# Kernel tuning notes

Measured on AMD Instinct MI355X. Metric: run time of the kernel, lower is better.

Reference implementation:

```python
import math
import jax, jax.numpy as jnp
import numpy as np

B, S, DIM, H = 16, 1024, 1024, 16
HD = DIM // H            # head_dim = 64
ROPE_DIM = HD // 2       # 32; per-axis rotary dim
FT = 32                  # ft_seq_len, FT*FT == S
PT = 16                  # pt_seq_len
THETA = 10000.0
EPS = 1e-6


def _rope_cos_sin():
    # freqs_for='lang'
    freqs = 1.0 / THETA ** (jnp.arange(0, ROPE_DIM, 2, dtype=jnp.float32) / ROPE_DIM)  # [ROPE_DIM//2]
    t = jnp.arange(FT, dtype=jnp.float32) / FT * PT                                    # [FT]
    fs = jnp.einsum('n,f->nf', t, freqs)                                               # [FT, ROPE_DIM//2]
    fs = jnp.repeat(fs, 2, axis=-1)                                                    # [FT, ROPE_DIM]
    fh = jnp.broadcast_to(fs[:, None, :], (FT, FT, ROPE_DIM))
    fw = jnp.broadcast_to(fs[None, :, :], (FT, FT, ROPE_DIM))
    f = jnp.concatenate([fh, fw], axis=-1).reshape(-1, 2 * ROPE_DIM)                   # [S, HD]
    return jnp.cos(f), jnp.sin(f)


def _rotate_half(x):
    x1, x2 = jnp.split(x, 2, axis=-1)
    return jnp.concatenate((-x2, x1), axis=-1)


def _rms_norm(x, w):
    xf = x.astype(jnp.float32)
    var = jnp.mean(jnp.square(xf), axis=-1, keepdims=True)
    return (w * (xf * jax.lax.rsqrt(var + EPS))).astype(x.dtype)


def setup_inputs() -> dict:
    key = jax.random.key(0)
    ks = jax.random.split(key, 4)
    sd = 1.0 / math.sqrt(DIM)
    return {
        'x': jax.random.normal(ks[0], (B, S, DIM), dtype=jnp.float32),
        'w_qkv': jax.random.normal(ks[1], (DIM, 3 * DIM), dtype=jnp.float32) * sd,
        'b_qkv': jnp.zeros((3 * DIM,), dtype=jnp.float32),
        'q_norm_w': jnp.ones((HD,), dtype=jnp.float32),
        'k_norm_w': jnp.ones((HD,), dtype=jnp.float32),
        'w_out': jax.random.normal(ks[2], (DIM, DIM), dtype=jnp.float32) * sd,
        'b_out': jnp.zeros((DIM,), dtype=jnp.float32),
    }


def reference(x, w_qkv, b_qkv, q_norm_w, k_norm_w, w_out, b_out):
    cos, sin = _rope_cos_sin()                    # [S, HD] each
    cos = cos[None, None].astype(x.dtype)
    sin = sin[None, None].astype(x.dtype)

    qkv = x @ w_qkv + b_qkv                       # [B,S,3*DIM]
    qkv = qkv.reshape(B, S, 3, H, HD).transpose(2, 0, 3, 1, 4)  # [3,B,H,S,HD]
    q, k, v = qkv[0], qkv[1], qkv[2]

    q = _rms_norm(q, q_norm_w)
    k = _rms_norm(k, k_norm_w)

    q = q * cos + _rotate_half(q) * sin
    k = k * cos + _rotate_half(k) * sin

    scale = 1.0 / math.sqrt(HD)
    logits = jnp.einsum('bhqd,bhkd->bhqk', q.astype(jnp.float32), k.astype(jnp.float32)) * scale
    attn = jax.nn.softmax(logits, axis=-1).astype(x.dtype)
    out = jnp.einsum('bhqk,bhkd->bhqd', attn, v)  # [B,H,S,HD]

    out = out.transpose(0, 2, 1, 3).reshape(B, S, DIM)
    return out @ w_out + b_out
```

## Files before the change

### kernel.cpp

```cpp
#include <hip/hip_runtime.h>
#include <cstdint>
#include <cstddef>

#define B_    16
#define S_    1024
#define DIM_  1024
#define H_    16
#define HD_   64
#define TDIM  3072

typedef unsigned short ushort_t;
typedef unsigned int   uint_t;
typedef __attribute__((ext_vector_type(8)))  short s8v;
typedef __attribute__((ext_vector_type(4)))  float f32x4;
typedef __attribute__((ext_vector_type(16))) float f32x16;

__device__ __forceinline__ float b2f(ushort_t u) {
    union { uint_t i; float f; } t; t.i = (uint_t)u << 16; return t.f;
}
__device__ __forceinline__ ushort_t f2b(float f) {
    union { float f; uint_t i; } t; t.f = f;
    uint_t r = t.i + 0x7FFFu + ((t.i >> 16) & 1u);
    return (ushort_t)(r >> 16);
}
__device__ __forceinline__ uint_t cvt_pk_bf16(float a, float b) {
    uint_t r;
    asm("v_cvt_pk_bf16_f32 %0, %1, %2" : "=v"(r) : "v"(a), "v"(b));
    return r;
}
__device__ __forceinline__ float max3f(float a, float b, float c) {
    float r;
    asm("v_max3_f32 %0, %1, %2, %3" : "=v"(r) : "v"(a), "v"(b), "v"(c));
    return r;
}

__device__ __forceinline__ f32x4 mfma_bf16(s8v a, s8v b, f32x4 c) {
    asm volatile("v_mfma_f32_16x16x32_bf16 %0, %1, %2, %0" : "+v"(c) : "v"(a), "v"(b));
    return c;
}
__device__ __forceinline__ f32x16 mfma32_bf16(s8v a, s8v b, f32x16 c) {
    asm volatile("v_mfma_f32_32x32x16_bf16 %0, %1, %2, %0" : "+v"(c) : "v"(a), "v"(b));
    return c;
}

__device__ __forceinline__ void gload16(const void* g, void* l) {
    __builtin_amdgcn_global_load_lds(
        (const __attribute__((address_space(1))) uint_t*)g,
        (__attribute__((address_space(3))) uint_t*)l, 16, 0, 0);
}

__device__ __forceinline__ void bar() {
    asm volatile("" ::: "memory");
    __builtin_amdgcn_s_barrier();
    asm volatile("" ::: "memory");
}
__device__ __forceinline__ void wait_vm0() {
    asm volatile("s_waitcnt vmcnt(0)" ::: "memory");
}
__device__ __forceinline__ void wait_vm4() {
    asm volatile("s_waitcnt vmcnt(4)" ::: "memory");
}

__global__ __launch_bounds__(256) void f32_to_bf16_vec(const float* __restrict__ src,
                                                       short* __restrict__ dst, int n8) {
    int i = blockIdx.x * 256 + threadIdx.x;
    if (i < n8) {
        float4 a = *(const float4*)(src + (size_t)i * 8);
        float4 b = *(const float4*)(src + (size_t)i * 8 + 4);
        s8v t;
        t[0] = (short)f2b(a.x); t[1] = (short)f2b(a.y);
        t[2] = (short)f2b(a.z); t[3] = (short)f2b(a.w);
        t[4] = (short)f2b(b.x); t[5] = (short)f2b(b.y);
        t[6] = (short)f2b(b.z); t[7] = (short)f2b(b.w);
        *(s8v*)(dst + (size_t)i * 8) = t;
    }
}

__global__ __launch_bounds__(256) void rope_tables(float* __restrict__ cos_t,
                                                   float* __restrict__ sin_t) {
    int idx = blockIdx.x * 256 + threadIdx.x;
    int s = idx >> 6;
    int d = idx & 63;
    int pos = (d < 32) ? (s >> 5) : (s & 31);
    int i   = (d & 31) >> 1;
    float freq  = expf(-(float)i * 0.5756462732485115f);
    float angle = (float)pos * 0.5f * freq;
    cos_t[idx] = cosf(angle);
    sin_t[idx] = sinf(angle);
}

__global__ __launch_bounds__(256) void transpose_to_bf16(const float* __restrict__ Wsrc,
                                                         short* __restrict__ WT,
                                                         int K, int N) {
    __shared__ float t[32][33];
    int tx = threadIdx.x & 31, ty = threadIdx.x >> 5;
    int n0 = blockIdx.x * 32, k0 = blockIdx.y * 32;
#pragma unroll
    for (int i = 0; i < 4; ++i)
        t[ty + 8 * i][tx] = Wsrc[(size_t)(k0 + ty + 8 * i) * N + n0 + tx];
    __syncthreads();
#pragma unroll
    for (int i = 0; i < 4; ++i)
        WT[(size_t)(n0 + ty + 8 * i) * K + k0 + tx] = (short)f2b(t[tx][ty + 8 * i]);
}

template<typename CT, bool NORM>
__global__ __launch_bounds__(512) void gemm8ph(
        const short* __restrict__ A, const short* __restrict__ BT,
        const float* __restrict__ bias, CT* __restrict__ C,
        int M, int N, int K, int NX,
        const float* __restrict__ qw, const float* __restrict__ kw,
        const float* __restrict__ cos_t, const float* __restrict__ sin_t) {
    __shared__ short As[2][256 * 64];
    __shared__ short Bs[3][256 * 64];

    const int tid  = threadIdx.x;
    const int w    = tid >> 6;
    const int lane = tid & 63;
    const int l15  = lane & 15, lg = lane >> 4;
    const int wm = w >> 2, wn = w & 3;

    const int nwg  = gridDim.x;
    const int cpx  = nwg >> 3;
    const int wgid = (blockIdx.x & 7) * cpx + (blockIdx.x >> 3);
    const int bx = wgid % NX, by = wgid / NX;
    const int m0 = by * 256, n0 = bx * 256;

    const int NT = K >> 6;

    const int sgrow = w * 8 + (lane >> 3);
    const int ksrc  = (((lane & 7) ^ (lane >> 3)) * 8);

    auto stageA = [&](int t, int buf) {
        const size_t k0 = (size_t)t * 64;
#pragma unroll
        for (int j = 0; j < 4; ++j)
            gload16(A + (size_t)(m0 + j * 64 + sgrow) * K + k0 + ksrc,
                    &As[buf][(j * 64 + w * 8) * 64]);
    };
    auto stageB = [&](int t, int buf) {
        const size_t k0 = (size_t)t * 64;
#pragma unroll
        for (int j = 0; j < 4; ++j)
            gload16(BT + (size_t)(n0 + j * 64 + sgrow) * K + k0 + ksrc,
                    &Bs[buf][(j * 64 + w * 8) * 64]);
    };

    const int swz = l15 & 7;

    auto rdA = [&](int buf, int mh, s8v (&dst)[4][2]) {
#pragma unroll
        for (int i = 0; i < 4; ++i) {
            int row = wm * 128 + mh * 64 + i * 16 + l15;
#pragma unroll
            for (int kk = 0; kk < 2; ++kk)
                dst[i][kk] = *(const s8v*)&As[buf][row * 64 + (((kk * 4 + lg) ^ swz) * 8)];
        }
    };
    auto rdB = [&](int buf, int nh, s8v (&dst)[4][2]) {
#pragma unroll
        for (int ni = 0; ni < 2; ++ni) {
            int row = wn * 64 + (nh * 2 + ni) * 16 + l15;
#pragma unroll
            for (int kk = 0; kk < 2; ++kk)
                dst[nh * 2 + ni][kk] = *(const s8v*)&Bs[buf][row * 64 + (((kk * 4 + lg) ^ swz) * 8)];
        }
    };

    stageA(0, 0);
    stageB(0, 0);
    stageB(1, 1);
    wait_vm4();
    bar();

    s8v a0[4][2], a1[4][2], bb[4][2];
    rdA(0, 0, a0);
    rdB(0, 0, bb);
    rdB(0, 1, bb);
    rdA(0, 1, a1);

    f32x4 acc[8][4] = {};

    int bufB = 0;
    for (int t = 0; t < NT; ++t) {
        const int bufA  = t & 1;
        const int nbufB = (bufB == 2) ? 0 : bufB + 1;
        const int sbufB = (nbufB == 2) ? 0 : nbufB + 1;

        if (t + 1 < NT) stageA(t + 1, bufA ^ 1);
        if (t + 2 < NT) stageB(t + 2, sbufB);

        __builtin_amdgcn_s_setprio(1);
#pragma unroll
        for (int i = 0; i < 4; ++i)
#pragma unroll
            for (int ni = 0; ni < 2; ++ni)
#pragma unroll
                for (int kk = 0; kk < 2; ++kk)
                    acc[i][ni] = mfma_bf16(a0[i][kk], bb[ni][kk], acc[i][ni]);
        __builtin_amdgcn_s_setprio(0);

        __builtin_amdgcn_s_setprio(1);
#pragma unroll
        for (int i = 0; i < 4; ++i)
#pragma unroll
            for (int ni = 2; ni < 4; ++ni)
#pragma unroll
                for (int kk = 0; kk < 2; ++kk)
                    acc[i][ni] = mfma_bf16(a0[i][kk], bb[ni][kk], acc[i][ni]);
        __builtin_amdgcn_s_setprio(0);

        __builtin_amdgcn_s_setprio(1);
#pragma unroll
        for (int i = 0; i < 4; ++i)
#pragma unroll
            for (int ni = 0; ni < 2; ++ni)
#pragma unroll
                for (int kk = 0; kk < 2; ++kk)
                    acc[4 + i][ni] = mfma_bf16(a1[i][kk], bb[ni][kk], acc[4 + i][ni]);
        __builtin_amdgcn_s_setprio(0);

        if (t < NT - 2) wait_vm4(); else wait_vm0();
        bar();

        if (t + 1 < NT) {
            rdA(bufA ^ 1, 0, a0);
            rdB(nbufB, 0, bb);
        }

        __builtin_amdgcn_s_setprio(1);
#pragma unroll
        for (int i = 0; i < 4; ++i)
#pragma unroll
            for (int ni = 2; ni < 4; ++ni)
#pragma unroll
                for (int kk = 0; kk < 2; ++kk)
                    acc[4 + i][ni] = mfma_bf16(a1[i][kk], bb[ni][kk], acc[4 + i][ni]);
        __builtin_amdgcn_s_setprio(0);

        if (t + 1 < NT) {
            rdB(nbufB, 1, bb);
            rdA(bufA ^ 1, 1, a1);
        }
        bufB = nbufB;
    }

    const int colbase = n0 + wn * 64;
    if constexpr (NORM) {
        if (colbase < 2048) {
            const float* nw = (colbase < 1024) ? qw : kw;
            float wv[4], bv[4];
#pragma unroll
            for (int ni = 0; ni < 4; ++ni) {
                wv[ni] = nw[16 * ni + l15];
                bv[ni] = bias[colbase + 16 * ni + l15];
            }
#pragma unroll
            for (int mi = 0; mi < 8; ++mi) {
#pragma unroll
                for (int r = 0; r < 4; ++r) {
                    int row = m0 + wm * 128 + mi * 16 + lg * 4 + r;
                    int s = row & (S_ - 1);
                    float v[4];
#pragma unroll
                    for (int ni = 0; ni < 4; ++ni) v[ni] = acc[mi][ni][r] + bv[ni];
                    float ss = v[0]*v[0] + v[1]*v[1] + v[2]*v[2] + v[3]*v[3];
                    ss += __shfl_xor(ss, 1);
                    ss += __shfl_xor(ss, 2);
                    ss += __shfl_xor(ss, 4);
                    ss += __shfl_xor(ss, 8);
                    float rms = rsqrtf(ss * (1.0f / 64.0f) + 1e-6f);
                    float xn[4];
#pragma unroll
                    for (int ni = 0; ni < 4; ++ni) xn[ni] = v[ni] * rms * wv[ni];
#pragma unroll
                    for (int ni = 0; ni < 4; ++ni) {
                        int d = 16 * ni + l15;
                        float c  = cos_t[s * 64 + d];
                        float sn = sin_t[s * 64 + d];
                        float rot = (ni < 2) ? -xn[ni + 2] : xn[ni - 2];
                        C[(size_t)row * N + colbase + d] = (short)f2b(xn[ni] * c + rot * sn);
                    }
                }
            }
            return;
        }
    }
#pragma unroll
    for (int ni = 0; ni < 4; ++ni) {
        float bvv = bias[colbase + 16 * ni + l15];
#pragma unroll
        for (int mi = 0; mi < 8; ++mi) {
#pragma unroll
            for (int r = 0; r < 4; ++r) {
                size_t row = (size_t)(m0 + wm * 128 + mi * 16 + lg * 4 + r);
                int    col = colbase + 16 * ni + l15;
                float v = acc[mi][ni][r] + bvv;
                if constexpr (sizeof(CT) == 4) C[row * N + col] = v;
                else                           C[row * N + col] = (short)f2b(v);
            }
        }
    }
}

__global__ __launch_bounds__(256) void attn_mfma(const short* __restrict__ qkv,
                                                 short* __restrict__ attn) {
    __shared__ ushort_t pool[9216];
    ushort_t* Ks = pool;
    ushort_t* Vt = pool + 4608;

    const float SC  = 0.18033688011112042f;
    const float THR = 11.0f;

    const int tid  = threadIdx.x;
    const int w    = tid >> 6;
    const int lane = tid & 63;
    const int l31  = lane & 31, l5 = lane >> 5;

    const int bid = blockIdx.x;
    const int xcd = bid & 7;
    const int jj_ = bid >> 3;
    const int bh  = xcd * 32 + (jj_ & 31);
    const int b   = bh >> 4, h = bh & 15;
    const int q0  = (jj_ >> 5) * 128;

    const short* qbase = qkv + (size_t)b * S_ * TDIM + h * HD_;
    const short* kb_ = qbase + DIM_;
    const short* vb_ = qbase + 2 * DIM_;

    s8v qf[4];
#pragma unroll
    for (int kc = 0; kc < 4; ++kc)
        qf[kc] = *(const s8v*)(qbase + (size_t)(q0 + w * 32 + l31) * TDIM + kc * 16 + l5 * 8);

    f32x16 of0 = {}, of1 = {};
    float m_s = -1e30f, l_s = 0.f;

    const int kr   = tid >> 3;
    const int kp8  = (tid & 7) * 8;
    const int vkp  = tid >> 3;
    const int va   = tid & 7;
    const int vp8  = va * 8;
    const int k2    = 2 * vkp;
    const int kperm = (k2 & 0x33) | ((k2 & 4) << 1) | ((k2 & 8) >> 1);
    const int vcol  = kperm ^ ((va & 3) << 4);
    const int vsw   = ((l31 >> 3) & 3) << 4;

    s8v kA, kB, vA, vB;
    auto prefetch = [&](int kt) {
        const short* kbt = kb_ + (size_t)kt * 64 * TDIM;
        const short* vbt = vb_ + (size_t)kt * 64 * TDIM;
        kA = *(const s8v*)(kbt + (size_t)kr * TDIM + kp8);
        kB = *(const s8v*)(kbt + (size_t)(kr + 32) * TDIM + kp8);
        vA = *(const s8v*)(vbt + (size_t)k2 * TDIM + vp8);
        vB = *(const s8v*)(vbt + (size_t)(k2 + 1) * TDIM + vp8);
    };
    prefetch(0);

    for (int kt = 0; kt < 16; ++kt) {
        *(s8v*)&Ks[kr * 72 + kp8]        = kA;
        *(s8v*)&Ks[(kr + 32) * 72 + kp8] = kB;
#pragma unroll
        for (int j = 0; j < 8; ++j) {
            uint_t pk = (ushort_t)vA[j] | ((uint_t)(ushort_t)vB[j] << 16);
            *(uint_t*)&Vt[(vp8 + j) * 72 + vcol] = pk;
        }
        __syncthreads();

        if (kt < 15) prefetch(kt + 1);

        f32x16 st0 = {}, st1 = {};
        __builtin_amdgcn_s_setprio(1);
#pragma unroll
        for (int kc = 0; kc < 4; ++kc) {
            s8v kf0 = *(const s8v*)&Ks[l31 * 72 + kc * 16 + l5 * 8];
            s8v kf1 = *(const s8v*)&Ks[(32 + l31) * 72 + kc * 16 + l5 * 8];
            st0 = mfma32_bf16(kf0, qf[kc], st0);
            st1 = mfma32_bf16(kf1, qf[kc], st1);
        }
        __builtin_amdgcn_s_setprio(0);

        float ma = fmaxf(st0[0], st1[0]);
        float mb = fmaxf(st0[8], st1[8]);
#pragma unroll
        for (int r = 1; r < 8; ++r) {
            ma = max3f(st0[r],     st1[r],     ma);
            mb = max3f(st0[8 + r], st1[8 + r], mb);
        }
        float mx = fmaxf(ma, mb);
        mx = fmaxf(mx, __shfl_xor(mx, 32));
        float mxs = mx * SC;

        if (!__all(mxs <= m_s + THR)) {
            float mnew  = fmaxf(m_s, mxs);
            float alpha = exp2f(m_s - mnew);
            m_s = mnew;
            l_s *= alpha;
#pragma unroll
            for (int r = 0; r < 16; ++r) { of0[r] *= alpha; of1[r] *= alpha; }
        }

        float la = 0.f, lb = 0.f, lc = 0.f, ld = 0.f;
#pragma unroll
        for (int r = 0; r < 16; r += 2) {
            float p00 = exp2f(__builtin_fmaf(st0[r],     SC, -m_s));
            float p01 = exp2f(__builtin_fmaf(st0[r + 1], SC, -m_s));
            float p10 = exp2f(__builtin_fmaf(st1[r],     SC, -m_s));
            float p11 = exp2f(__builtin_fmaf(st1[r + 1], SC, -m_s));
            st0[r] = p00; st0[r + 1] = p01;
            st1[r] = p10; st1[r + 1] = p11;
            la += p00; lb += p01; lc += p10; ld += p11;
        }
        float ls = (la + lb) + (lc + ld);
        ls += __shfl_xor(ls, 32);
        l_s += ls;

        uint_t P20[8], P21[8];
#pragma unroll
        for (int i = 0; i < 8; ++i) {
            P20[i] = cvt_pk_bf16(st0[2 * i], st0[2 * i + 1]);
            P21[i] = cvt_pk_bf16(st1[2 * i], st1[2 * i + 1]);
        }

        __builtin_amdgcn_s_setprio(1);
#pragma unroll
        for (int kb = 0; kb < 2; ++kb) {
            const uint_t* P2 = kb ? P21 : P20;
#pragma unroll
            for (int c = 0; c < 2; ++c) {
                union { uint_t u[4]; s8v v; } pf;
                pf.u[0] = P2[4 * c + 0];
                pf.u[1] = P2[4 * c + 1];
                pf.u[2] = P2[4 * c + 2];
                pf.u[3] = P2[4 * c + 3];

                int kcol = (kb * 32 + c * 16 + l5 * 8) ^ vsw;
                s8v vf0 = *(const s8v*)&Vt[l31 * 72 + kcol];
                s8v vf1 = *(const s8v*)&Vt[(32 + l31) * 72 + kcol];
                of0 = mfma32_bf16(vf0, pf.v, of0);
                of1 = mfma32_bf16(vf1, pf.v, of1);
            }
        }
        __builtin_amdgcn_s_setprio(0);
        __syncthreads();
    }

    float inv = 1.0f / l_s;
    ushort_t* OL = pool + w * 2304;
#pragma unroll
    for (int r = 0; r < 16; ++r) {
        int d = (r & 3) + 8 * (r >> 2) + 4 * l5;
        OL[l31 * 72 + d]      = f2b(of0[r] * inv);
        OL[l31 * 72 + 32 + d] = f2b(of1[r] * inv);
    }
#pragma unroll
    for (int i = 0; i < 4; ++i) {
        int idx = lane + i * 64;
        int row = idx >> 3, ch = idx & 7;
        *(s8v*)&attn[((size_t)b * S_ + q0 + w * 32 + row) * DIM_ + h * HD_ + ch * 8] =
            *(const s8v*)&OL[row * 72 + ch * 8];
    }
}

extern "C" void kernel_launch(void* const* d_in, const int* in_sizes, int n_in,
                              void* d_out, int out_size, void* d_ws, size_t ws_size,
                              hipStream_t stream) {
    const float* x        = (const float*)d_in[0];
    const float* w_qkv    = (const float*)d_in[1];
    const float* b_qkv    = (const float*)d_in[2];
    const float* q_norm_w = (const float*)d_in[3];
    const float* k_norm_w = (const float*)d_in[4];
    const float* w_out    = (const float*)d_in[5];
    const float* b_out    = (const float*)d_in[6];
    float* out = (float*)d_out;

    const size_t OFF_QKV = 0;
    const size_t OFF_ATT = 100663296;
    const size_t OFF_XB  = OFF_ATT + 33554432;
    const size_t OFF_WQ  = OFF_XB + 33554432;
    const size_t OFF_WO  = OFF_WQ + 6291456;
    const size_t OFF_CT  = OFF_WO + 2097152;
    const size_t OFF_ST  = OFF_CT + 262144;
    const size_t NEED    = OFF_ST + 262144;

    if (ws_size < NEED) {
        hipMemsetAsync(d_out, 0, (size_t)out_size * sizeof(float), stream);
        return;
    }

    char* ws = (char*)d_ws;
    short* qkv   = (short*)(ws + OFF_QKV);
    short* attnb = (short*)(ws + OFF_ATT);
    short* xb    = (short*)(ws + OFF_XB);
    short* wqkvT = (short*)(ws + OFF_WQ);
    short* woutT = (short*)(ws + OFF_WO);
    float* cos_t = (float*)(ws + OFF_CT);
    float* sin_t = (float*)(ws + OFF_ST);

    rope_tables<<<dim3(256), dim3(256), 0, stream>>>(cos_t, sin_t);
    f32_to_bf16_vec<<<dim3(8192), dim3(256), 0, stream>>>(x, xb, 2097152);
    transpose_to_bf16<<<dim3(96, 32), dim3(256), 0, stream>>>(w_qkv, wqkvT, 1024, 3072);
    transpose_to_bf16<<<dim3(32, 32), dim3(256), 0, stream>>>(w_out, woutT, 1024, 1024);

    gemm8ph<short, true><<<dim3(768), dim3(512), 0, stream>>>(
        xb, wqkvT, b_qkv, qkv, 16384, 3072, 1024, 12,
        q_norm_w, k_norm_w, cos_t, sin_t);

    attn_mfma<<<dim3(2048), dim3(256), 0, stream>>>(qkv, attnb);

    gemm8ph<float, false><<<dim3(256), dim3(512), 0, stream>>>(
        attnb, woutT, b_out, out, 16384, 1024, 1024, 4,
        nullptr, nullptr, nullptr, nullptr);
}
```

Before: 296.5 us.

## Double-buffer K/V tiles in LDS for attention and widen row pitch

The attention kernel now keeps two LDS buffers for the K and transposed V tiles. The next tile's prefetched registers are written into the alternate buffer after the PV MFMAs, so each iteration needs one barrier instead of two. The LDS row pitch also changes from 72 to 76 elements, which alters bank mapping but makes 16-byte row accesses no longer 16-byte aligned. LDS use roughly doubles, which may reduce occupancy, and the XOR swizzle was tuned for the old pitch.

```diff
diff --git a/kernel.cpp b/kernel.cpp
--- a/kernel.cpp
+++ b/kernel.cpp
@@ -303,11 +303,13 @@
     }
 }
 
+#define PITCH 76
+#define HBUF  (64 * PITCH)
+#define BUFSZ (2 * HBUF)
+
 __global__ __launch_bounds__(256) void attn_mfma(const short* __restrict__ qkv,
                                                  short* __restrict__ attn) {
-    __shared__ ushort_t pool[9216];
-    ushort_t* Ks = pool;
-    ushort_t* Vt = pool + 4608;
+    __shared__ ushort_t pool[2 * BUFSZ];
 
     const float SC  = 0.18033688011112042f;
     const float THR = 11.0f;
@@ -355,17 +357,25 @@
         vA = *(const s8v*)(vbt + (size_t)k2 * TDIM + vp8);
         vB = *(const s8v*)(vbt + (size_t)(k2 + 1) * TDIM + vp8);
     };
-    prefetch(0);
-
-    for (int kt = 0; kt < 16; ++kt) {
-        *(s8v*)&Ks[kr * 72 + kp8]        = kA;
-        *(s8v*)&Ks[(kr + 32) * 72 + kp8] = kB;
+    auto write_tile = [&](ushort_t* base) {
+        ushort_t* Kw = base;
+        ushort_t* Vw = base + HBUF;
+        *(s8v*)&Kw[kr * PITCH + kp8]        = kA;
+        *(s8v*)&Kw[(kr + 32) * PITCH + kp8] = kB;
 #pragma unroll
         for (int j = 0; j < 8; ++j) {
             uint_t pk = (ushort_t)vA[j] | ((uint_t)(ushort_t)vB[j] << 16);
-            *(uint_t*)&Vt[(vp8 + j) * 72 + vcol] = pk;
-        }
-        __syncthreads();
+            *(uint_t*)&Vw[(vp8 + j) * PITCH + vcol] = pk;
+        }
+    };
+
+    prefetch(0);
+    write_tile(pool);
+    __syncthreads();
+
+    for (int kt = 0; kt < 16; ++kt) {
+        ushort_t* Kb = pool + (kt & 1) * BUFSZ;
+        ushort_t* Vb = Kb + HBUF;
 
         if (kt < 15) prefetch(kt + 1);
 
@@ -373,8 +383,8 @@
         __builtin_amdgcn_s_setprio(1);
 #pragma unroll
         for (int kc = 0; kc < 4; ++kc) {
-            s8v kf0 = *(const s8v*)&Ks[l31 * 72 + kc * 16 + l5 * 8];
-            s8v kf1 = *(const s8v*)&Ks[(32 + l31) * 72 + kc * 16 + l5 * 8];
+            s8v kf0 = *(const s8v*)&Kb[l31 * PITCH + kc * 16 + l5 * 8];
+            s8v kf1 = *(const s8v*)&Kb[(32 + l31) * PITCH + kc * 16 + l5 * 8];
             st0 = mfma32_bf16(kf0, qf[kc], st0);
             st1 = mfma32_bf16(kf1, qf[kc], st1);
         }
@@ -435,30 +445,32 @@
                 pf.u[3] = P2[4 * c + 3];
 
                 int kcol = (kb * 32 + c * 16 + l5 * 8) ^ vsw;
-                s8v vf0 = *(const s8v*)&Vt[l31 * 72 + kcol];
-                s8v vf1 = *(const s8v*)&Vt[(32 + l31) * 72 + kcol];
+                s8v vf0 = *(const s8v*)&Vb[l31 * PITCH + kcol];
+                s8v vf1 = *(const s8v*)&Vb[(32 + l31) * PITCH + kcol];
                 of0 = mfma32_bf16(vf0, pf.v, of0);
                 of1 = mfma32_bf16(vf1, pf.v, of1);
             }
         }
         __builtin_amdgcn_s_setprio(0);
+
+        if (kt < 15) write_tile(pool + ((kt + 1) & 1) * BUFSZ);
         __syncthreads();
     }
 
     float inv = 1.0f / l_s;
-    ushort_t* OL = pool + w * 2304;
+    ushort_t* OL = pool + w * 32 * PITCH;
 #pragma unroll
     for (int r = 0; r < 16; ++r) {
         int d = (r & 3) + 8 * (r >> 2) + 4 * l5;
-        OL[l31 * 72 + d]      = f2b(of0[r] * inv);
-        OL[l31 * 72 + 32 + d] = f2b(of1[r] * inv);
+        OL[l31 * PITCH + d]      = f2b(of0[r] * inv);
+        OL[l31 * PITCH + 32 + d] = f2b(of1[r] * inv);
     }
 #pragma unroll
     for (int i = 0; i < 4; ++i) {
         int idx = lane + i * 64;
         int row = idx >> 3, ch = idx & 7;
         *(s8v*)&attn[((size_t)b * S_ + q0 + w * 32 + row) * DIM_ + h * HD_ + ch * 8] =
-            *(const s8v*)&OL[row * 72 + ch * 8];
+            *(const s8v*)&OL[row * PITCH + ch * 8];
     }
 }
 
```

Result: slower. 443.1 us (+49.5%).
